# Optimization experiments

Hardware: AMD Instinct MI355X
Metric: run time of the kernel (lower is better)

The kernel has to match this reference:

```python
import jax, jax.numpy as jnp
import numpy as np

K = 3                # k_const
NUM_CLASSES = 10
CLASS_SIZE = 5000
NUM_TRAIN = NUM_CLASSES * CLASS_SIZE   # 50000
DIGIT_WIDTH = 256
NUM_TEST = 4096


def setup_inputs() -> dict:
    key = jax.random.key(0)
    k1, k2 = jax.random.split(key)
    training_set = jax.random.randint(k1, (NUM_TRAIN, DIGIT_WIDTH), 0, 2, dtype=jnp.int32)
    test_set = jax.random.randint(k2, (NUM_TEST, DIGIT_WIDTH), 0, 2, dtype=jnp.int32)
    return {"training_set": training_set, "test_set": test_set}


def reference(training_set, test_set):
    # Hamming distance between binary vectors a,b: sum(a XOR b)
    # = sum(a) + sum(b) - 2*dot(a,b); computed as one int matmul instead of
    # materializing the [T, N, D] XOR tensor.
    tr_sum = jnp.sum(training_set, axis=1)                    # [N]
    te_sum = jnp.sum(test_set, axis=1)                        # [T]
    inner = jnp.matmul(test_set, training_set.T)              # [T, N] int32
    dists = te_sum[:, None] + tr_sum[None, :] - 2 * inner     # [T, N]

    # Original loop keeps the K smallest distances, ties won by the earlier
    # training index (strict '<' insertion). lax.top_k on negated distances
    # breaks ties by smaller index, matching that behavior.
    _, knn_idx = jax.lax.top_k(-dists, K)                     # [T, K]
    labels = knn_idx // CLASS_SIZE                            # [T, K]

    # Majority vote per test sample; argmax returns first max on ties,
    # same as torch.argmax in the original.
    T = test_set.shape[0]
    votes = jnp.zeros((T, NUM_CLASSES), dtype=jnp.int32)
    votes = votes.at[jnp.arange(T)[:, None], labels].add(1)   # [T, C]
    return jnp.argmax(votes, axis=1)                          # [T]
```

## Files before the change

### kernel.cpp

```cpp
#include <hip/hip_runtime.h>
#include <stdint.h>

typedef unsigned long long u64;
typedef unsigned int u32;
typedef int v4i  __attribute__((ext_vector_type(4)));
typedef int v16i __attribute__((ext_vector_type(16)));

#define NUM_TRAIN   50000
#define NUM_TEST    4096
#define CLASS_SIZE  5000
#define TRAIN_PAD   50176
#define TOT_TILES   1568

#define SZ_TRAIN   ((size_t)TRAIN_PAD * 256)
#define SZ_TEST    ((size_t)NUM_TEST * 256)
#define SZ_TESUM   ((size_t)NUM_TEST * 4)
#define OFF_TEST   (SZ_TRAIN)
#define OFF_TESUM  (OFF_TEST + SZ_TEST)
#define OFF_PART   (OFF_TESUM + SZ_TESUM)
#define WS_NEED(NCH) (OFF_PART + (size_t)NUM_TEST * (NCH) * 3 * 4)

__device__ __forceinline__ void insert3(u32& k0, u32& k1, u32& k2, u32 key) {
    u32 m1, m2;
    asm("v_med3_u32 %0, %1, %2, %3" : "=v"(m1) : "v"(k0), "v"(k1), "v"(key));
    asm("v_med3_u32 %0, %1, %2, %3" : "=v"(m2) : "v"(k1), "v"(k2), "v"(key));
    k0 = min(k0, key);
    k1 = m1; k2 = m2;
}
__device__ __forceinline__ void merge3(u32& a0, u32& a1, u32& a2,
                                       u32 b0, u32 b1, u32 b2) {
    u32 hi0 = max(a0, b0);
    u32 lo1 = min(a1, b1);
    u32 c0  = min(a0, b0);
    u32 c1  = min(hi0, lo1);
    u32 c2  = min(max(lo1, hi0), min(a2, b2));
    a0 = c0; a1 = c1; a2 = c2;
}
__device__ __forceinline__ int wave_sum(int s) {
    #pragma unroll
    for (int off = 1; off < 64; off <<= 1) s += __shfl_xor(s, off);
    return s;
}

__global__ __launch_bounds__(256) void pack_all(const int* __restrict__ train,
                                                const int* __restrict__ test,
                                                char* __restrict__ dstA,
                                                char* __restrict__ dstB,
                                                int* __restrict__ tesum) {
    int r    = (blockIdx.x * 256 + threadIdx.x) >> 6;
    int lane = threadIdx.x & 63;
    if (r < TRAIN_PAD) {
        int4 v = make_int4(0, 0, 0, 0);
        if (r < NUM_TRAIN)
            v = *reinterpret_cast<const int4*>(train + (size_t)r * 256 + lane * 4);
        u32 w = (u32)(v.x & 1) | ((u32)(v.y & 1) << 8)
              | ((u32)(v.z & 1) << 16) | ((u32)(v.w & 1) << 24);
        *reinterpret_cast<u32*>(dstA + (size_t)r * 256 + lane * 4) = w;
    } else {
        int rt = r - TRAIN_PAD;
        int4 v = *reinterpret_cast<const int4*>(test + (size_t)rt * 256 + lane * 4);
        u32 w = (u32)((1 - 2 * v.x) & 0xFF) | ((u32)((1 - 2 * v.y) & 0xFF) << 8)
              | ((u32)((1 - 2 * v.z) & 0xFF) << 16) | ((u32)((1 - 2 * v.w) & 0xFF) << 24);
        *reinterpret_cast<u32*>(dstB + (size_t)rt * 256 + lane * 4) = w;
        int total = wave_sum(v.x + v.y + v.z + v.w);
        if (lane == 0) tesum[rt] = total;
    }
}

template<int NCH>
__global__ __launch_bounds__(256) void mfma_knn(const char* __restrict__ A,
                                                const char* __restrict__ Bt,
                                                const int* __restrict__ tesum,
                                                u32* __restrict__ partial) {
    constexpr int TILES  = TOT_TILES / NCH;
    constexpr int CHROWS = TRAIN_PAD / NCH;
    static_assert((TILES & 1) == 0, "2-phase dbuf loop needs even TILES");
    const int cg   = blockIdx.x / NCH;
    const int c    = blockIdx.x % NCH;
    const int tid  = threadIdx.x;
    const int wid  = tid >> 6;
    const int lane = tid & 63;
    const int a    = lane & 31;
    const int kh   = lane >> 5;

    const int col0 = cg * 256 + wid * 64 + a;
    const int col1 = col0 + 32;
    v4i bf0[8], bf1[8];
    {
        const char* bp0 = Bt + (size_t)col0 * 256 + kh * 16;
        const char* bp1 = Bt + (size_t)col1 * 256 + kh * 16;
        #pragma unroll
        for (int kk = 0; kk < 8; ++kk) {
            bf0[kk] = *reinterpret_cast<const v4i*>(bp0 + kk * 32);
            bf1[kk] = *reinterpret_cast<const v4i*>(bp1 + kk * 32);
        }
    }
    const u32 base0 = ((u32)tesum[col0] << 16);
    const u32 base1 = ((u32)tesum[col1] << 16);

    __shared__ char lds[2][8192];
    char* rd[8];
    #pragma unroll
    for (int kk = 0; kk < 8; ++kk)
        rd[kk] = &lds[0][kk * 1024 + kh * 512 + ((a ^ kk) & 31) * 16];

    const int grow = tid >> 3, gc = tid & 7;
    const char* gsrc0 = A + (size_t)c * CHROWS * 256 + grow * 256 + gc * 32;
    char* w0 = &lds[0][gc * 1024 +       ((grow ^ gc) & 31) * 16];
    char* w1 = &lds[0][gc * 1024 + 512 + ((grow ^ gc) & 31) * 16];

    u32 p00 = 0x7FFFFFFFu, p01 = 0x7FFFFFFFu, p02 = 0x7FFFFFFFu;
    u32 p10 = 0x7FFFFFFFu, p11 = 0x7FFFFFFFu, p12 = 0x7FFFFFFFu;

    {
        uint4 s0 = *reinterpret_cast<const uint4*>(gsrc0);
        uint4 s1 = *reinterpret_cast<const uint4*>(gsrc0 + 16);
        *reinterpret_cast<uint4*>(w0) = s0;
        *reinterpret_cast<uint4*>(w1) = s1;
    }
    __syncthreads();

#define TILE_STEP(TT, RB, WB)                                                 \
    {                                                                         \
        const int tt = (TT);                                                  \
        uint4 s0, s1;                                                         \
        const bool pf = (tt + 1 < TILES);                                     \
        if (pf) {                                                             \
            const char* g = gsrc0 + (size_t)(tt + 1) * 8192;                  \
            s0 = *reinterpret_cast<const uint4*>(g);                          \
            s1 = *reinterpret_cast<const uint4*>(g + 16);                     \
        }                                                                     \
        v16i acc0 = {0,0,0,0,0,0,0,0,0,0,0,0,0,0,0,0};                        \
        v16i acc1 = {0,0,0,0,0,0,0,0,0,0,0,0,0,0,0,0};                        \
        __builtin_amdgcn_s_setprio(1);                                        \
        _Pragma("unroll")                                                     \
        for (int kk = 0; kk < 8; ++kk) {                                      \
            v4i af = *reinterpret_cast<const v4i*>(rd[kk] + (RB) * 8192);     \
            acc0 = __builtin_amdgcn_mfma_i32_32x32x32_i8(af, bf0[kk], acc0, 0, 0, 0); \
            acc1 = __builtin_amdgcn_mfma_i32_32x32x32_i8(af, bf1[kk], acc1, 0, 0, 0); \
        }                                                                     \
        __builtin_amdgcn_s_setprio(0);                                        \
        const int tbase = c * CHROWS + tt * 32;                               \
        const u32 kb0 = base0 + (u32)(tbase + 4 * kh);                        \
        const u32 kb1 = base1 + (u32)(tbase + 4 * kh);                        \
        if (tbase + 32 <= NUM_TRAIN) {                                        \
            _Pragma("unroll")                                                 \
            for (int g = 0; g < 16; ++g) {                                    \
                const int row = (g & 3) + 8 * (g >> 2);                       \
                insert3(p00, p01, p02, ((u32)acc0[g] << 16) + kb0 + (u32)row);\
                insert3(p10, p11, p12, ((u32)acc1[g] << 16) + kb1 + (u32)row);\
            }                                                                 \
        } else {                                                              \
            _Pragma("unroll")                                                 \
            for (int g = 0; g < 16; ++g) {                                    \
                const int row = (g & 3) + 8 * (g >> 2);                       \
                const int idx = tbase + 4 * kh + row;                         \
                u32 key0 = (idx < NUM_TRAIN)                                  \
                    ? (((u32)acc0[g] << 16) + kb0 + (u32)row) : 0xFFFFFFFFu;  \
                u32 key1 = (idx < NUM_TRAIN)                                  \
                    ? (((u32)acc1[g] << 16) + kb1 + (u32)row) : 0xFFFFFFFFu;  \
                insert3(p00, p01, p02, key0);                                 \
                insert3(p10, p11, p12, key1);                                 \
            }                                                                 \
        }                                                                     \
        if (pf) {                                                             \
            *reinterpret_cast<uint4*>(w0 + (WB) * 8192) = s0;                 \
            *reinterpret_cast<uint4*>(w1 + (WB) * 8192) = s1;                 \
        }                                                                     \
        __syncthreads();                                                      \
    }

    #pragma unroll 1
    for (int t = 0; t < TILES; t += 2) {
        TILE_STEP(t,     0, 1);
        TILE_STEP(t + 1, 1, 0);
    }
#undef TILE_STEP

    u32 o0, o1, o2;
    o0 = __shfl_xor(p00, 32); o1 = __shfl_xor(p01, 32); o2 = __shfl_xor(p02, 32);
    merge3(p00, p01, p02, o0, o1, o2);
    o0 = __shfl_xor(p10, 32); o1 = __shfl_xor(p11, 32); o2 = __shfl_xor(p12, 32);
    merge3(p10, p11, p12, o0, o1, o2);
    if (kh == 0) {
        u32* d0 = partial + ((size_t)c * NUM_TEST + col0) * 3;
        d0[0] = p00; d0[1] = p01; d0[2] = p02;
        u32* d1 = partial + ((size_t)c * NUM_TEST + col1) * 3;
        d1[0] = p10; d1[1] = p11; d1[2] = p12;
    }
}

template<int NCH>
__global__ __launch_bounds__(256) void vote_knn16(const u32* __restrict__ partial,
                                                  int* __restrict__ out) {
    static_assert(NCH % 16 == 0, "16-lane vote needs NCH % 16 == 0");
    const int gid = blockIdx.x * 256 + threadIdx.x;
    const int t   = gid >> 4;
    const int sub = gid & 15;
    if (t >= NUM_TEST) return;
    u32 a0 = 0x7FFFFFFFu, a1 = 0x7FFFFFFFu, a2 = 0x7FFFFFFFu;
    #pragma unroll
    for (int j = 0; j < NCH / 16; ++j) {
        const int c = sub + 16 * j;
        const u32* q = partial + ((size_t)c * NUM_TEST + t) * 3;
        merge3(a0, a1, a2, q[0], q[1], q[2]);
    }
    #pragma unroll
    for (int off = 1; off < 16; off <<= 1) {
        u32 o0 = __shfl_xor(a0, off);
        u32 o1 = __shfl_xor(a1, off);
        u32 o2 = __shfl_xor(a2, off);
        merge3(a0, a1, a2, o0, o1, o2);
    }
    if (sub == 0) {
        const int l0 = (int)(a0 & 0xFFFFu) / CLASS_SIZE;
        const int l1 = (int)(a1 & 0xFFFFu) / CLASS_SIZE;
        const int l2 = (int)(a2 & 0xFFFFu) / CLASS_SIZE;
        int winner;
        if (l0 == l1 || l0 == l2)      winner = l0;
        else if (l1 == l2)             winner = l1;
        else winner = min(l0, min(l1, l2));
        out[t] = winner;
    }
}

#define TT          8
#define NCHUNK      4
#define CHUNK_ROWS  (NUM_TRAIN / NCHUNK)

__device__ __forceinline__ void insert3_minmax(u32& k0, u32& k1, u32& k2, u32 key) {
    u32 m0 = min(k0, key);
    u32 m1 = min(k1, max(k0, key));
    u32 m2 = min(k2, max(k1, key));
    k0 = m0; k1 = m1; k2 = m2;
}

__global__ void pack_kernel(const int* __restrict__ train,
                            const int* __restrict__ test,
                            u64* __restrict__ packed) {
    int wave = (blockIdx.x * blockDim.x + threadIdx.x) >> 6;
    int lane = threadIdx.x & 63;
    const int* src = (wave < NUM_TRAIN)
                       ? (train + (size_t)wave * 256)
                       : (test + (size_t)(wave - NUM_TRAIN) * 256);
    int4 v = *reinterpret_cast<const int4*>(src + lane * 4);
    u64 b0 = __ballot(v.x & 1);
    u64 b1 = __ballot(v.y & 1);
    u64 b2 = __ballot(v.z & 1);
    u64 b3 = __ballot(v.w & 1);
    if (lane == 0) {
        u64* dst = packed + (size_t)wave * 4;
        dst[0] = b0; dst[1] = b1; dst[2] = b2; dst[3] = b3;
    }
}

__global__ __launch_bounds__(256) void knn_kernel(const u32* __restrict__ packed,
                                                  u32* __restrict__ partial) {
    const int g    = blockIdx.x >> 2;
    const int c    = blockIdx.x & 3;
    const int tid  = threadIdx.x;
    const int base = g * TT;
    const uint4* rows  = (const uint4*)packed;
    const u32*  testp  = packed + (size_t)NUM_TRAIN * 8;

    u32 te[TT][8];
    #pragma unroll
    for (int s = 0; s < TT; ++s) {
        const u32* p = testp + (size_t)(base + s) * 8;
        #pragma unroll
        for (int j = 0; j < 8; ++j) te[s][j] = p[j];
    }
    u32 k0[TT], k1[TT], k2[TT];
    #pragma unroll
    for (int s = 0; s < TT; ++s) { k0[s] = k1[s] = k2[s] = 0x7FFFFFFFu; }

    const int start = c * CHUNK_ROWS;
    const int end   = start + CHUNK_ROWS;
    for (int r = start + tid; r < end; r += 256) {
        uint4 a0 = rows[(size_t)r * 2];
        uint4 a1 = rows[(size_t)r * 2 + 1];
        #pragma unroll
        for (int s = 0; s < TT; ++s) {
            int d = __popc(a0.x ^ te[s][0]);
            d += __popc(a0.y ^ te[s][1]);
            d += __popc(a0.z ^ te[s][2]);
            d += __popc(a0.w ^ te[s][3]);
            d += __popc(a1.x ^ te[s][4]);
            d += __popc(a1.y ^ te[s][5]);
            d += __popc(a1.z ^ te[s][6]);
            d += __popc(a1.w ^ te[s][7]);
            u32 key = ((u32)d << 16) | (u32)r;
            insert3_minmax(k0[s], k1[s], k2[s], key);
        }
    }
    #pragma unroll
    for (int s = 0; s < TT; ++s) {
        for (int off = 1; off < 64; off <<= 1) {
            u32 o0 = __shfl_xor(k0[s], off);
            u32 o1 = __shfl_xor(k1[s], off);
            u32 o2 = __shfl_xor(k2[s], off);
            merge3(k0[s], k1[s], k2[s], o0, o1, o2);
        }
    }
    __shared__ u32 red[4][TT][3];
    const int wave = tid >> 6, lane = tid & 63;
    if (lane == 0) {
        #pragma unroll
        for (int s = 0; s < TT; ++s) {
            red[wave][s][0] = k0[s];
            red[wave][s][1] = k1[s];
            red[wave][s][2] = k2[s];
        }
    }
    __syncthreads();
    if (tid < TT) {
        const int s = tid;
        u32 a0 = red[0][s][0], a1 = red[0][s][1], a2 = red[0][s][2];
        #pragma unroll
        for (int w = 1; w < 4; ++w)
            merge3(a0, a1, a2, red[w][s][0], red[w][s][1], red[w][s][2]);
        u32* dst = partial + ((size_t)(base + s) * NCHUNK + c) * 3;
        dst[0] = a0; dst[1] = a1; dst[2] = a2;
    }
}

__global__ __launch_bounds__(256) void merge_kernel(const u32* __restrict__ partial,
                                                    int* __restrict__ out) {
    int t = blockIdx.x * blockDim.x + threadIdx.x;
    if (t >= NUM_TEST) return;
    const u32* p = partial + (size_t)t * NCHUNK * 3;
    u32 a0 = p[0], a1 = p[1], a2 = p[2];
    #pragma unroll
    for (int c = 1; c < NCHUNK; ++c)
        merge3(a0, a1, a2, p[c * 3 + 0], p[c * 3 + 1], p[c * 3 + 2]);
    const int l0 = (int)(a0 & 0xFFFFu) / CLASS_SIZE;
    const int l1 = (int)(a1 & 0xFFFFu) / CLASS_SIZE;
    const int l2 = (int)(a2 & 0xFFFFu) / CLASS_SIZE;
    int winner;
    if (l0 == l1 || l0 == l2)      winner = l0;
    else if (l1 == l2)             winner = l1;
    else winner = min(l0, min(l1, l2));
    out[t] = winner;
}

extern "C" void kernel_launch(void* const* d_in, const int* in_sizes, int n_in,
                              void* d_out, int out_size, void* d_ws, size_t ws_size,
                              hipStream_t stream) {
    const int* train = (const int*)d_in[0];
    const int* test  = (const int*)d_in[1];
    int* out = (int*)d_out;

    if (ws_size >= WS_NEED(112)) {
        char* train_i8 = (char*)d_ws;
        char* test_i8  = (char*)d_ws + OFF_TEST;
        int*  tesum    = (int*)((char*)d_ws + OFF_TESUM);
        u32*  partial  = (u32*)((char*)d_ws + OFF_PART);

        pack_all<<<(TRAIN_PAD + NUM_TEST) / 4, 256, 0, stream>>>(train, test,
                                                                 train_i8, test_i8, tesum);
        mfma_knn<112><<<16 * 112, 256, 0, stream>>>(train_i8, test_i8, tesum, partial);
        vote_knn16<112><<<(NUM_TEST * 16) / 256, 256, 0, stream>>>(partial, out);
    } else {
        u64* packed = (u64*)d_ws;
        u32* partial = (u32*)((char*)d_ws + (size_t)(NUM_TRAIN + NUM_TEST) * 4 * sizeof(u64));
        const int total_rows = NUM_TRAIN + NUM_TEST;
        pack_kernel<<<total_rows / 4, 256, 0, stream>>>(train, test, packed);
        knn_kernel<<<(NUM_TEST / TT) * NCHUNK, 256, 0, stream>>>((const u32*)packed, partial);
        merge_kernel<<<(NUM_TEST + 255) / 256, 256, 0, stream>>>(partial, out);
    }
}
```

Baseline: 78.59 us.

## Halve per-wave test columns and use fewer, longer train chunks

Each wave now handles 32 test columns with one MFMA accumulator instead of 64 with two, so blocks cover 128 test samples and the grid has 32 column groups. The train dimension is split into 56 chunks instead of 112, so each block loops over more tiles and writes fewer partial top-3 results, and the vote kernel merges 8 chunks per lane group. Launch bounds request 8 blocks per CU to raise occupancy from the lower register use. The trade-off is that each LDS A-tile now feeds half as many MFMAs, which doubles LDS and global reads of the train set per unit of compute.

```diff
diff --git a/kernel.cpp b/kernel.cpp
--- a/kernel.cpp
+++ b/kernel.cpp
@@ -68,10 +68,10 @@
 }
 
 template<int NCH>
-__global__ __launch_bounds__(256) void mfma_knn(const char* __restrict__ A,
-                                                const char* __restrict__ Bt,
-                                                const int* __restrict__ tesum,
-                                                u32* __restrict__ partial) {
+__global__ __launch_bounds__(256, 8) void mfma_knn(const char* __restrict__ A,
+                                                   const char* __restrict__ Bt,
+                                                   const int* __restrict__ tesum,
+                                                   u32* __restrict__ partial) {
     constexpr int TILES  = TOT_TILES / NCH;
     constexpr int CHROWS = TRAIN_PAD / NCH;
     static_assert((TILES & 1) == 0, "2-phase dbuf loop needs even TILES");
@@ -83,26 +83,22 @@
     const int a    = lane & 31;
     const int kh   = lane >> 5;
 
-    const int col0 = cg * 256 + wid * 64 + a;
-    const int col1 = col0 + 32;
-    v4i bf0[8], bf1[8];
+    const int col0 = cg * 128 + wid * 32 + a;
+    v4i bf[8];
     {
-        const char* bp0 = Bt + (size_t)col0 * 256 + kh * 16;
-        const char* bp1 = Bt + (size_t)col1 * 256 + kh * 16;
-        #pragma unroll
-        for (int kk = 0; kk < 8; ++kk) {
-            bf0[kk] = *reinterpret_cast<const v4i*>(bp0 + kk * 32);
-            bf1[kk] = *reinterpret_cast<const v4i*>(bp1 + kk * 32);
-        }
+        const char* bp = Bt + (size_t)col0 * 256 + kh * 16;
+        #pragma unroll
+        for (int kk = 0; kk < 8; ++kk)
+            bf[kk] = *reinterpret_cast<const v4i*>(bp + kk * 32);
     }
     const u32 base0 = ((u32)tesum[col0] << 16);
-    const u32 base1 = ((u32)tesum[col1] << 16);
 
     __shared__ char lds[2][8192];
-    char* rd[8];
+    u32 rdo[8];
     #pragma unroll
     for (int kk = 0; kk < 8; ++kk)
-        rd[kk] = &lds[0][kk * 1024 + kh * 512 + ((a ^ kk) & 31) * 16];
+        rdo[kk] = kk * 1024 + kh * 512 + ((a ^ kk) & 31) * 16;
+    const char* lds0 = &lds[0][0];
 
     const int grow = tid >> 3, gc = tid & 7;
     const char* gsrc0 = A + (size_t)c * CHROWS * 256 + grow * 256 + gc * 32;
@@ -110,7 +106,6 @@
     char* w1 = &lds[0][gc * 1024 + 512 + ((grow ^ gc) & 31) * 16];
 
     u32 p00 = 0x7FFFFFFFu, p01 = 0x7FFFFFFFu, p02 = 0x7FFFFFFFu;
-    u32 p10 = 0x7FFFFFFFu, p11 = 0x7FFFFFFFu, p12 = 0x7FFFFFFFu;
 
     {
         uint4 s0 = *reinterpret_cast<const uint4*>(gsrc0);
@@ -130,25 +125,21 @@
             s0 = *reinterpret_cast<const uint4*>(g);                          \
             s1 = *reinterpret_cast<const uint4*>(g + 16);                     \
         }                                                                     \
-        v16i acc0 = {0,0,0,0,0,0,0,0,0,0,0,0,0,0,0,0};                        \
-        v16i acc1 = {0,0,0,0,0,0,0,0,0,0,0,0,0,0,0,0};                        \
+        v16i acc = {0,0,0,0,0,0,0,0,0,0,0,0,0,0,0,0};                         \
         __builtin_amdgcn_s_setprio(1);                                        \
         _Pragma("unroll")                                                     \
         for (int kk = 0; kk < 8; ++kk) {                                      \
-            v4i af = *reinterpret_cast<const v4i*>(rd[kk] + (RB) * 8192);     \
-            acc0 = __builtin_amdgcn_mfma_i32_32x32x32_i8(af, bf0[kk], acc0, 0, 0, 0); \
-            acc1 = __builtin_amdgcn_mfma_i32_32x32x32_i8(af, bf1[kk], acc1, 0, 0, 0); \
+            v4i af = *reinterpret_cast<const v4i*>(lds0 + rdo[kk] + (RB) * 8192); \
+            acc = __builtin_amdgcn_mfma_i32_32x32x32_i8(af, bf[kk], acc, 0, 0, 0); \
         }                                                                     \
         __builtin_amdgcn_s_setprio(0);                                        \
         const int tbase = c * CHROWS + tt * 32;                               \
         const u32 kb0 = base0 + (u32)(tbase + 4 * kh);                        \
-        const u32 kb1 = base1 + (u32)(tbase + 4 * kh);                        \
         if (tbase + 32 <= NUM_TRAIN) {                                        \
             _Pragma("unroll")                                                 \
             for (int g = 0; g < 16; ++g) {                                    \
                 const int row = (g & 3) + 8 * (g >> 2);                       \
-                insert3(p00, p01, p02, ((u32)acc0[g] << 16) + kb0 + (u32)row);\
-                insert3(p10, p11, p12, ((u32)acc1[g] << 16) + kb1 + (u32)row);\
+                insert3(p00, p01, p02, ((u32)acc[g] << 16) + kb0 + (u32)row); \
             }                                                                 \
         } else {                                                              \
             _Pragma("unroll")                                                 \
@@ -156,11 +147,8 @@
                 const int row = (g & 3) + 8 * (g >> 2);                       \
                 const int idx = tbase + 4 * kh + row;                         \
                 u32 key0 = (idx < NUM_TRAIN)                                  \
-                    ? (((u32)acc0[g] << 16) + kb0 + (u32)row) : 0xFFFFFFFFu;  \
-                u32 key1 = (idx < NUM_TRAIN)                                  \
-                    ? (((u32)acc1[g] << 16) + kb1 + (u32)row) : 0xFFFFFFFFu;  \
+                    ? (((u32)acc[g] << 16) + kb0 + (u32)row) : 0xFFFFFFFFu;   \
                 insert3(p00, p01, p02, key0);                                 \
-                insert3(p10, p11, p12, key1);                                 \
             }                                                                 \
         }                                                                     \
         if (pf) {                                                             \
@@ -180,33 +168,29 @@
     u32 o0, o1, o2;
     o0 = __shfl_xor(p00, 32); o1 = __shfl_xor(p01, 32); o2 = __shfl_xor(p02, 32);
     merge3(p00, p01, p02, o0, o1, o2);
-    o0 = __shfl_xor(p10, 32); o1 = __shfl_xor(p11, 32); o2 = __shfl_xor(p12, 32);
-    merge3(p10, p11, p12, o0, o1, o2);
     if (kh == 0) {
         u32* d0 = partial + ((size_t)c * NUM_TEST + col0) * 3;
         d0[0] = p00; d0[1] = p01; d0[2] = p02;
-        u32* d1 = partial + ((size_t)c * NUM_TEST + col1) * 3;
-        d1[0] = p10; d1[1] = p11; d1[2] = p12;
     }
 }
 
 template<int NCH>
-__global__ __launch_bounds__(256) void vote_knn16(const u32* __restrict__ partial,
-                                                  int* __restrict__ out) {
-    static_assert(NCH % 16 == 0, "16-lane vote needs NCH % 16 == 0");
+__global__ __launch_bounds__(256) void vote_knn8(const u32* __restrict__ partial,
+                                                 int* __restrict__ out) {
+    static_assert(NCH % 8 == 0, "8-lane vote needs NCH % 8 == 0");
     const int gid = blockIdx.x * 256 + threadIdx.x;
-    const int t   = gid >> 4;
-    const int sub = gid & 15;
+    const int t   = gid >> 3;
+    const int sub = gid & 7;
     if (t >= NUM_TEST) return;
     u32 a0 = 0x7FFFFFFFu, a1 = 0x7FFFFFFFu, a2 = 0x7FFFFFFFu;
     #pragma unroll
-    for (int j = 0; j < NCH / 16; ++j) {
-        const int c = sub + 16 * j;
+    for (int j = 0; j < NCH / 8; ++j) {
+        const int c = sub + 8 * j;
         const u32* q = partial + ((size_t)c * NUM_TEST + t) * 3;
         merge3(a0, a1, a2, q[0], q[1], q[2]);
     }
     #pragma unroll
-    for (int off = 1; off < 16; off <<= 1) {
+    for (int off = 1; off < 8; off <<= 1) {
         u32 o0 = __shfl_xor(a0, off);
         u32 o1 = __shfl_xor(a1, off);
         u32 o2 = __shfl_xor(a2, off);
@@ -350,7 +334,7 @@
     const int* test  = (const int*)d_in[1];
     int* out = (int*)d_out;
 
-    if (ws_size >= WS_NEED(112)) {
+    if (ws_size >= WS_NEED(56)) {
         char* train_i8 = (char*)d_ws;
         char* test_i8  = (char*)d_ws + OFF_TEST;
         int*  tesum    = (int*)((char*)d_ws + OFF_TESUM);
@@ -358,8 +342,8 @@
 
         pack_all<<<(TRAIN_PAD + NUM_TEST) / 4, 256, 0, stream>>>(train, test,
                                                                  train_i8, test_i8, tesum);
-        mfma_knn<112><<<16 * 112, 256, 0, stream>>>(train_i8, test_i8, tesum, partial);
-        vote_knn16<112><<<(NUM_TEST * 16) / 256, 256, 0, stream>>>(partial, out);
+        mfma_knn<56><<<32 * 56, 256, 0, stream>>>(train_i8, test_i8, tesum, partial);
+        vote_knn8<56><<<(NUM_TEST * 8) / 256, 256, 0, stream>>>(partial, out);
     } else {
         u64* packed = (u64*)d_ws;
         u32* partial = (u32*)((char*)d_ws + (size_t)(NUM_TRAIN + NUM_TEST) * 4 * sizeof(u64));
```

Result: slower. 228.6 us (+190.9%).
